# Performance work log

Measured on AMD Instinct MI355X. Metric: run time of the kernel, lower is better.

Reference implementation:

```python
import jax, jax.numpy as jnp
import numpy as np

E = 16          # expert_num
T = 8192        # token_num
H = 1024        # hidden_size
I = 4096        # intermediate_size
LN_EPS = 1e-12


def setup_inputs() -> dict:
    key = jax.random.key(0)
    ks = jax.random.split(key, 6)
    hidden_states = jax.random.normal(ks[0], (T, H), dtype=jnp.float32)
    perm = jax.random.permutation(ks[1], T).astype(jnp.int32)
    s1 = 1.0 / np.sqrt(H)
    s2 = 1.0 / np.sqrt(I)
    w1 = jax.random.uniform(ks[2], (E, I, H), jnp.float32, -s1, s1)
    b1 = jax.random.uniform(ks[3], (E, I), jnp.float32, -s1, s1)
    w2 = jax.random.uniform(ks[4], (E, H, I), jnp.float32, -s2, s2)
    b2 = jax.random.uniform(ks[5], (E, H), jnp.float32, -s2, s2)
    ln_gamma = jnp.ones((H,), jnp.float32)
    ln_beta = jnp.zeros((H,), jnp.float32)
    return {"hidden_states": hidden_states, "perm": perm, "w1": w1, "b1": b1,
            "w2": w2, "b2": b2, "ln_gamma": ln_gamma, "ln_beta": ln_beta}


def _layer_norm(x, gamma, beta, eps):
    mu = jnp.mean(x, axis=-1, keepdims=True)
    var = jnp.var(x, axis=-1, keepdims=True)
    return (x - mu) * jax.lax.rsqrt(var + eps) * gamma + beta


def reference(hidden_states, perm, w1, b1, w2, b2, ln_gamma, ln_beta):
    # dispatch: gather tokens by random permutation, group per expert
    xp = hidden_states[perm].reshape(E, T // E, H)            # [E, T/E, H]
    # grouped expert FFN (batched GEMM replaces the per-expert Python loop)
    h = jnp.einsum('eth,eih->eti', xp, w1) + b1[:, None, :]   # [E, T/E, I]
    h = jax.nn.gelu(h, approximate=False)
    o = jnp.einsum('eti,ehi->eth', h, w2) + b2[:, None, :]    # [E, T/E, H]
    # scatter-restore via inverse permutation
    restore = jnp.argsort(perm)
    o = o.reshape(T, H)[restore]
    # dropout is identity (p=0, eval); residual + LayerNorm
    return _layer_norm(o + hidden_states, ln_gamma, ln_beta, LN_EPS)
```

## Files before the change

kernel.cpp:

```cpp
#include <hip/hip_runtime.h>
#include <hip/hip_bf16.h>
#include <stdint.h>

#define E_NUM 16
#define T_NUM 8192
#define H_DIM 1024
#define I_DIM 4096
#define MPE   512

typedef __attribute__((ext_vector_type(8))) short short8;
typedef __attribute__((ext_vector_type(4))) float f32x4;
using bf16 = __hip_bfloat16;

typedef const __attribute__((address_space(1))) void GLV;
typedef __attribute__((address_space(3))) void LDSV;

__device__ __forceinline__ uint32_t pack2_bf16(float a, float b) {
  union { float f; uint32_t u; } ua, ub;
  ua.f = a; ub.f = b;
  uint32_t x = ua.u + (0x7FFFu + ((ua.u >> 16) & 1u));
  uint32_t y = ub.u + (0x7FFFu + ((ub.u >> 16) & 1u));
  return (x >> 16) | (y & 0xFFFF0000u);
}

__device__ __forceinline__ short8 cvt8(f32x4 a, f32x4 b) {
  union { short8 s; __hip_bfloat162 h[4]; } r;
  r.h[0] = __float22bfloat162_rn({a[0], a[1]});
  r.h[1] = __float22bfloat162_rn({a[2], a[3]});
  r.h[2] = __float22bfloat162_rn({b[0], b[1]});
  r.h[3] = __float22bfloat162_rn({b[2], b[3]});
  return r.s;
}

__device__ __forceinline__ float fast_gelu(float x) {
  const float p = x * fmaf(x * x, -0.0713548162726f, -1.59576912161f);
  return x * __builtin_amdgcn_rcpf(1.0f + __expf(p));
}

__global__ __launch_bounds__(256)
void gather_cast_kernel(const float* __restrict__ hs, const int* __restrict__ perm,
                        uint32_t* __restrict__ xp) {
  const int r = blockIdx.x;
  const int t = threadIdx.x;
  const int src = perm[r];
  float4 v = ((const float4*)(hs + (size_t)src * H_DIM))[t];
  uint2 o;
  o.x = pack2_bf16(v.x, v.y);
  o.y = pack2_bf16(v.z, v.w);
  ((uint2*)(xp + (size_t)r * (H_DIM / 2)))[t] = o;
}

template<int EPI, int KSPLIT, int N, int KFULL, int KLEN, int LOG_NBN>
__global__ __launch_bounds__(1024, 4)
void moe_gemm_kernel(const bf16* __restrict__ A, const float* __restrict__ Bw,
                     const float* __restrict__ bias, bf16* __restrict__ Hout,
                     float* __restrict__ Pout) {
  constexpr int NK = KLEN / 32;
  __shared__ bf16  As[3][512 * 32];
  __shared__ float Bs[3][128 * 32];

  const int nwg = gridDim.x, qx = nwg >> 3, orig = blockIdx.x;
  const int wg = (orig & 7) * qx + (orig >> 3);
  const int bn   = wg & ((1 << LOG_NBN) - 1);
  const int rest = wg >> LOG_NBN;
  const int ks = (KSPLIT == 2) ? (rest & 1) : 0;
  const int e  = (KSPLIT == 2) ? (rest >> 1) : rest;
  const int K0 = ks * KLEN;

  const int tid = threadIdx.x;
  const int l = tid & 63;
  const int w = tid >> 6;
  const int wr = w >> 1, wc = w & 1;
  const int fr = l & 15, fq = l >> 4;
  const int rx = fr & 7;

  const bf16*  Ae = A  + (size_t)e * MPE * KFULL + K0;
  const float* Be = Bw + ((size_t)e * N + (size_t)bn * 128) * KFULL + K0;

  const int apq = tid >> 3;
  const int ag  = (tid & 7) ^ (apq & 7);
  const bf16* As0 = Ae + (size_t)(apq       + 256 * (ag >> 2)) * KFULL + (ag & 3) * 8;
  const bf16* As1 = Ae + (size_t)(apq + 128 + 256 * (ag >> 2)) * KFULL + (ag & 3) * 8;

  const float* Bsrc = Be + (size_t)(tid >> 3) * KFULL + ((tid & 7) ^ ((tid >> 3) & 7)) * 4;

  const int aso = (((((wr >> 2) << 2)) | fq) ^ rx) * 8;
  const int bp0 = (((fq << 1))     ^ rx) * 4;
  const int bp1 = (((fq << 1) | 1) ^ rx) * 4;

#define STAGE(buf, kt)                                                              \
  {                                                                                 \
    __builtin_amdgcn_global_load_lds((GLV*)(As0 + (kt) * 32),                       \
                                     (LDSV*)&As[buf][tid * 8], 16, 0, 0);           \
    __builtin_amdgcn_global_load_lds((GLV*)(As1 + (kt) * 32),                       \
                                     (LDSV*)&As[buf][(1024 + tid) * 8], 16, 0, 0);  \
    __builtin_amdgcn_global_load_lds((GLV*)(Bsrc + (kt) * 32),                      \
                                     (LDSV*)&Bs[buf][tid * 4], 16, 0, 0);           \
  }

  f32x4 acc[4][4];
#pragma unroll
  for (int m = 0; m < 4; ++m)
#pragma unroll
    for (int n = 0; n < 4; ++n) acc[m][n] = (f32x4){0.f, 0.f, 0.f, 0.f};

  STAGE(0, 0);
  STAGE(1, 1);
  asm volatile("s_waitcnt vmcnt(3)" ::: "memory");
  __builtin_amdgcn_sched_barrier(0);
  __builtin_amdgcn_s_barrier();
  __builtin_amdgcn_sched_barrier(0);

  int bufc = 0, bufn1 = 1, bufn2 = 2;
  for (int t = 0; t < NK; ++t) {
    if (t + 2 < NK) STAGE(bufn2, t + 2);

    short8 a8[4];
#pragma unroll
    for (int m = 0; m < 4; ++m)
      a8[m] = *(const short8*)&As[bufc][((wr & 3) * 64 + m * 16 + fr) * 64 + aso];

#pragma unroll
    for (int n = 0; n < 4; ++n) {
      const int col = wc * 64 + n * 16 + fr;
      const f32x4 x0 = *(const f32x4*)&Bs[bufc][col * 32 + bp0];
      const f32x4 x1 = *(const f32x4*)&Bs[bufc][col * 32 + bp1];
      const short8 b8 = cvt8(x0, x1);
#pragma unroll
      for (int m = 0; m < 4; ++m)
        acc[m][n] = __builtin_amdgcn_mfma_f32_16x16x32_bf16(a8[m], b8, acc[m][n], 0, 0, 0);
    }

    if (t + 2 < NK) {
      asm volatile("s_waitcnt vmcnt(3)" ::: "memory");
      __builtin_amdgcn_sched_barrier(0);
      __builtin_amdgcn_s_barrier();
      __builtin_amdgcn_sched_barrier(0);
    } else if (t + 1 < NK) {
      asm volatile("s_waitcnt vmcnt(0)" ::: "memory");
      __builtin_amdgcn_sched_barrier(0);
      __builtin_amdgcn_s_barrier();
      __builtin_amdgcn_sched_barrier(0);
    }

    const int b0 = bufc;
    bufc = bufn1; bufn1 = bufn2; bufn2 = b0;
  }
#undef STAGE
  __syncthreads();

  if (EPI == 1) {
    float bv[4];
#pragma unroll
    for (int n = 0; n < 4; ++n)
      bv[n] = bias[(size_t)e * N + bn * 128 + wc * 64 + n * 16 + fr];
    bf16* He = Hout + (size_t)e * MPE * N;

    bf16* Ls = &As[0][0];
#pragma unroll
    for (int P = 0; P < 2; ++P) {
      if ((wr >> 2) == P) {
        const int wrl = wr & 3;
#pragma unroll
        for (int m = 0; m < 4; ++m) {
#pragma unroll
          for (int j = 0; j < 4; ++j) {
            const int lr = wrl * 64 + m * 16 + fq * 4 + j;
#pragma unroll
            for (int n = 0; n < 4; ++n) {
              const int c = wc * 64 + n * 16 + fr;
              const int byteoff = lr * 256 + ((c * 2) ^ ((lr & 7) << 4));
              Ls[byteoff >> 1] = __float2bfloat16(fast_gelu(acc[m][n][j] + bv[n]));
            }
          }
        }
      }
      __syncthreads();
#pragma unroll
      for (int q = 0; q < 4; ++q) {
        const int o = (tid + q * 1024) * 16;
        const int lr = o >> 8;
        const int cb = o & 255;
        const int sb = lr * 256 + (cb ^ ((lr & 7) << 4));
        uint4 v = *(const uint4*)((const char*)Ls + sb);
        *(uint4*)&He[(size_t)(P * 256 + lr) * N + bn * 128 + (cb >> 1)] = v;
      }
      __syncthreads();
    }
  } else {
    float* Pd = Pout + (size_t)ks * T_NUM * H_DIM + (size_t)e * MPE * N;
#pragma unroll
    for (int m = 0; m < 4; ++m) {
#pragma unroll
      for (int j = 0; j < 4; ++j) {
        const int row = wr * 64 + m * 16 + fq * 4 + j;
#pragma unroll
        for (int n = 0; n < 4; ++n) {
          const int col = bn * 128 + wc * 64 + n * 16 + fr;
          Pd[(size_t)row * N + col] = acc[m][n][j];
        }
      }
    }
  }
}

__global__ __launch_bounds__(256)
void ln_resid2_kernel(float* __restrict__ out, const float* __restrict__ hs,
                      const float* __restrict__ p0, const float* __restrict__ p1,
                      const float* __restrict__ b2, const float* __restrict__ gamma,
                      const float* __restrict__ beta, const int* __restrict__ perm,
                      const int two) {
  const int r = blockIdx.x;
  const int t = threadIdx.x;
  const int e = r >> 9;
  const int drow = perm[r];
  float4 a = ((const float4*)(p0 + (size_t)r * H_DIM))[t];
  if (two) {
    float4 b = ((const float4*)(p1 + (size_t)r * H_DIM))[t];
    a.x += b.x; a.y += b.y; a.z += b.z; a.w += b.w;
  }
  float4 bb = ((const float4*)(b2 + (size_t)e * H_DIM))[t];
  float4 h  = ((const float4*)(hs + (size_t)drow * H_DIM))[t];
  float v0 = a.x + bb.x + h.x, v1 = a.y + bb.y + h.y;
  float v2 = a.z + bb.z + h.z, v3 = a.w + bb.w + h.w;
  float s  = v0 + v1 + v2 + v3;
  float sq = v0 * v0 + v1 * v1 + v2 * v2 + v3 * v3;
#pragma unroll
  for (int off = 32; off > 0; off >>= 1) {
    s  += __shfl_down(s, off);
    sq += __shfl_down(sq, off);
  }
  __shared__ float ss[4], ssq[4];
  const int wv = t >> 6;
  if ((t & 63) == 0) { ss[wv] = s; ssq[wv] = sq; }
  __syncthreads();
  s  = ss[0] + ss[1] + ss[2] + ss[3];
  sq = ssq[0] + ssq[1] + ssq[2] + ssq[3];
  const float mu  = s * (1.0f / (float)H_DIM);
  const float var = sq * (1.0f / (float)H_DIM) - mu * mu;
  const float rs  = rsqrtf(var + 1e-12f);
  float4 g = ((const float4*)gamma)[t];
  float4 b = ((const float4*)beta)[t];
  float4 rr;
  rr.x = (v0 - mu) * rs * g.x + b.x;
  rr.y = (v1 - mu) * rs * g.y + b.y;
  rr.z = (v2 - mu) * rs * g.z + b.z;
  rr.w = (v3 - mu) * rs * g.w + b.w;
  ((float4*)(out + (size_t)drow * H_DIM))[t] = rr;
}

extern "C" void kernel_launch(void* const* d_in, const int* in_sizes, int n_in,
                              void* d_out, int out_size, void* d_ws, size_t ws_size,
                              hipStream_t stream) {
  const float* hs    = (const float*)d_in[0];
  const int*   perm  = (const int*)d_in[1];
  const float* w1    = (const float*)d_in[2];
  const float* b1    = (const float*)d_in[3];
  const float* w2    = (const float*)d_in[4];
  const float* b2    = (const float*)d_in[5];
  const float* gamma = (const float*)d_in[6];
  const float* beta  = (const float*)d_in[7];
  float* out = (float*)d_out;

  const size_t xp_b   = (size_t)T_NUM * H_DIM * sizeof(bf16);
  const size_t hbuf_b = (size_t)T_NUM * I_DIM * sizeof(bf16);
  const size_t part_b = (size_t)T_NUM * H_DIM * sizeof(float);

  bf16*  xp   = (bf16*)d_ws;
  bf16*  hbuf = (bf16*)((char*)d_ws + xp_b);
  float* pbuf = (float*)((char*)d_ws + xp_b + hbuf_b);

  gather_cast_kernel<<<T_NUM, 256, 0, stream>>>(hs, perm, (uint32_t*)xp);

  moe_gemm_kernel<1, 1, I_DIM, H_DIM, H_DIM, 5>
      <<<512, 1024, 0, stream>>>(xp, w1, b1, hbuf, nullptr);

  if (ws_size >= xp_b + hbuf_b + 2 * part_b) {
    moe_gemm_kernel<0, 2, H_DIM, I_DIM, I_DIM / 2, 3>
        <<<256, 1024, 0, stream>>>(hbuf, w2, nullptr, nullptr, pbuf);
    ln_resid2_kernel<<<T_NUM, 256, 0, stream>>>(out, hs, pbuf, pbuf + (size_t)T_NUM * H_DIM,
                                                b2, gamma, beta, perm, 1);
  } else {
    moe_gemm_kernel<0, 1, H_DIM, I_DIM, I_DIM, 3>
        <<<128, 1024, 0, stream>>>(hbuf, w2, nullptr, nullptr, pbuf);
    ln_resid2_kernel<<<T_NUM, 256, 0, stream>>>(out, hs, pbuf, nullptr,
                                                b2, gamma, beta, perm, 0);
  }
}
```

Before: 316.7 us.

## Convert fp32 weights to bf16 once when staging into LDS instead of per-wave

The weight tile no longer goes global-to-LDS as fp32 with every wave converting on read. Each thread now loads a float4 into registers, converts it to bf16 and writes it into a swizzled bf16 LDS layout. Waves then read ready-made short8 fragments. This halves the LDS footprint and read traffic for the weights and removes the repeated conversions from the MFMA loop. In exchange it adds register staging with alternating buffers, a VGPR round-trip and an extra lgkmcnt wait per iteration, and it loses the async direct-to-LDS path for the weights.

```diff
diff --git a/kernel.cpp b/kernel.cpp
--- a/kernel.cpp
+++ b/kernel.cpp
@@ -23,13 +23,11 @@
   return (x >> 16) | (y & 0xFFFF0000u);
 }
 
-__device__ __forceinline__ short8 cvt8(f32x4 a, f32x4 b) {
-  union { short8 s; __hip_bfloat162 h[4]; } r;
-  r.h[0] = __float22bfloat162_rn({a[0], a[1]});
-  r.h[1] = __float22bfloat162_rn({a[2], a[3]});
-  r.h[2] = __float22bfloat162_rn({b[0], b[1]});
-  r.h[3] = __float22bfloat162_rn({b[2], b[3]});
-  return r.s;
+__device__ __forceinline__ uint2 cvt4u(float4 a) {
+  union { uint2 u; __hip_bfloat162 h[2]; } r;
+  r.h[0] = __float22bfloat162_rn({a.x, a.y});
+  r.h[1] = __float22bfloat162_rn({a.z, a.w});
+  return r.u;
 }
 
 __device__ __forceinline__ float fast_gelu(float x) {
@@ -56,8 +54,8 @@
                      const float* __restrict__ bias, bf16* __restrict__ Hout,
                      float* __restrict__ Pout) {
   constexpr int NK = KLEN / 32;
-  __shared__ bf16  As[3][512 * 32];
-  __shared__ float Bs[3][128 * 32];
+  __shared__ bf16 As[3][512 * 32];
+  __shared__ bf16 Bs[3][64 * 64];
 
   const int nwg = gridDim.x, qx = nwg >> 3, orig = blockIdx.x;
   const int wg = (orig & 7) * qx + (orig >> 3);
@@ -82,71 +80,83 @@
   const bf16* As0 = Ae + (size_t)(apq       + 256 * (ag >> 2)) * KFULL + (ag & 3) * 8;
   const bf16* As1 = Ae + (size_t)(apq + 128 + 256 * (ag >> 2)) * KFULL + (ag & 3) * 8;
 
-  const float* Bsrc = Be + (size_t)(tid >> 3) * KFULL + ((tid & 7) ^ ((tid >> 3) & 7)) * 4;
+  const int bc = tid >> 3, bsg = tid & 7;
+  const float* Bsrc = Be + (size_t)bc * KFULL + bsg * 4;
+  const int bp  = bc & 63;
+  const int bwo = bp * 64 + (((((bc >> 6) << 2) | (bsg >> 1)) ^ (bp & 7)) << 3)
+                + (bsg & 1) * 4;
 
   const int aso = (((((wr >> 2) << 2)) | fq) ^ rx) * 8;
-  const int bp0 = (((fq << 1))     ^ rx) * 4;
-  const int bp1 = (((fq << 1) | 1) ^ rx) * 4;
-
-#define STAGE(buf, kt)                                                              \
+  const int bro = fr * 64 + ((((wc << 2) | fq) ^ rx) << 3);
+
+  f32x4 acc[4][4];
+#pragma unroll
+  for (int m = 0; m < 4; ++m)
+#pragma unroll
+    for (int n = 0; n < 4; ++n) acc[m][n] = (f32x4){0.f, 0.f, 0.f, 0.f};
+
+  float4 s0, s1;
+
+#define ISSUE_A(buf, kt)                                                            \
   {                                                                                 \
     __builtin_amdgcn_global_load_lds((GLV*)(As0 + (kt) * 32),                       \
                                      (LDSV*)&As[buf][tid * 8], 16, 0, 0);           \
     __builtin_amdgcn_global_load_lds((GLV*)(As1 + (kt) * 32),                       \
                                      (LDSV*)&As[buf][(1024 + tid) * 8], 16, 0, 0);  \
-    __builtin_amdgcn_global_load_lds((GLV*)(Bsrc + (kt) * 32),                      \
-                                     (LDSV*)&Bs[buf][tid * 4], 16, 0, 0);           \
-  }
-
-  f32x4 acc[4][4];
-#pragma unroll
-  for (int m = 0; m < 4; ++m)
-#pragma unroll
-    for (int n = 0; n < 4; ++n) acc[m][n] = (f32x4){0.f, 0.f, 0.f, 0.f};
-
-  STAGE(0, 0);
-  STAGE(1, 1);
+  }
+#define ISSUE_B(dst, kt)  { dst = *(const float4*)(Bsrc + (kt) * 32); }
+#define WRITE_B(buf, src) { *(uint2*)&Bs[buf][bwo] = cvt4u(src); }
+
+  ISSUE_A(0, 0); ISSUE_B(s0, 0);
+  ISSUE_A(1, 1); ISSUE_B(s1, 1);
   asm volatile("s_waitcnt vmcnt(3)" ::: "memory");
+  __builtin_amdgcn_sched_barrier(0);
+  WRITE_B(0, s0);
+  asm volatile("s_waitcnt lgkmcnt(0)" ::: "memory");
   __builtin_amdgcn_sched_barrier(0);
   __builtin_amdgcn_s_barrier();
   __builtin_amdgcn_sched_barrier(0);
 
   int bufc = 0, bufn1 = 1, bufn2 = 2;
   for (int t = 0; t < NK; ++t) {
-    if (t + 2 < NK) STAGE(bufn2, t + 2);
+    if (t + 2 < NK) {
+      ISSUE_A(bufn2, t + 2);
+      if ((t & 1) == 0) { ISSUE_B(s0, t + 2); } else { ISSUE_B(s1, t + 2); }
+      asm volatile("s_waitcnt vmcnt(3)" ::: "memory");
+      __builtin_amdgcn_sched_barrier(0);
+    } else {
+      asm volatile("s_waitcnt vmcnt(0)" ::: "memory");
+      __builtin_amdgcn_sched_barrier(0);
+    }
+    if (t + 1 < NK) {
+      if ((t & 1) == 0) { WRITE_B(bufn1, s1); } else { WRITE_B(bufn1, s0); }
+    }
 
     short8 a8[4];
 #pragma unroll
     for (int m = 0; m < 4; ++m)
       a8[m] = *(const short8*)&As[bufc][((wr & 3) * 64 + m * 16 + fr) * 64 + aso];
-
-#pragma unroll
-    for (int n = 0; n < 4; ++n) {
-      const int col = wc * 64 + n * 16 + fr;
-      const f32x4 x0 = *(const f32x4*)&Bs[bufc][col * 32 + bp0];
-      const f32x4 x1 = *(const f32x4*)&Bs[bufc][col * 32 + bp1];
-      const short8 b8 = cvt8(x0, x1);
-#pragma unroll
-      for (int m = 0; m < 4; ++m)
-        acc[m][n] = __builtin_amdgcn_mfma_f32_16x16x32_bf16(a8[m], b8, acc[m][n], 0, 0, 0);
-    }
-
-    if (t + 2 < NK) {
-      asm volatile("s_waitcnt vmcnt(3)" ::: "memory");
-      __builtin_amdgcn_sched_barrier(0);
-      __builtin_amdgcn_s_barrier();
-      __builtin_amdgcn_sched_barrier(0);
-    } else if (t + 1 < NK) {
-      asm volatile("s_waitcnt vmcnt(0)" ::: "memory");
-      __builtin_amdgcn_sched_barrier(0);
-      __builtin_amdgcn_s_barrier();
-      __builtin_amdgcn_sched_barrier(0);
-    }
+    short8 b8[4];
+#pragma unroll
+    for (int n = 0; n < 4; ++n)
+      b8[n] = *(const short8*)&Bs[bufc][bro + n * 1024];
+#pragma unroll
+    for (int m = 0; m < 4; ++m)
+#pragma unroll
+      for (int n = 0; n < 4; ++n)
+        acc[m][n] = __builtin_amdgcn_mfma_f32_16x16x32_bf16(a8[m], b8[n], acc[m][n], 0, 0, 0);
+
+    asm volatile("s_waitcnt lgkmcnt(0)" ::: "memory");
+    __builtin_amdgcn_sched_barrier(0);
+    __builtin_amdgcn_s_barrier();
+    __builtin_amdgcn_sched_barrier(0);
 
     const int b0 = bufc;
     bufc = bufn1; bufn1 = bufn2; bufn2 = b0;
   }
-#undef STAGE
+#undef ISSUE_A
+#undef ISSUE_B
+#undef WRITE_B
   __syncthreads();
 
   if (EPI == 1) {
```

After: 320.6 us. About the same (+1.2%).
